# Kernel optimization log

Measured on AMD Instinct MI355X. Metric: run time of the kernel, lower is better.

The kernel has to match this reference:

```python
import jax, jax.numpy as jnp
import numpy as np

B, S, D = 4, 2048, 256
H, RANK, DFF = 8, 8, 1024
DK = D // H
EPS = 1e-5


def _linear(x, W, b):
    # torch nn.Linear: y = x @ W.T + b, W shape (out, in)
    return jnp.einsum('bsd,od->bso', x, W) + b


def _layer_norm(x, g, b):
    mu = jnp.mean(x, axis=-1, keepdims=True)
    var = jnp.var(x, axis=-1, keepdims=True)
    return (x - mu) * jax.lax.rsqrt(var + EPS) * g + b


def setup_inputs() -> dict:
    key = jax.random.key(0)
    ks = jax.random.split(key, 20)
    r = RANK * H
    s = lambda fan_in: 1.0 / np.sqrt(fan_in)
    inp = {
        'x': jax.random.normal(ks[0], (B, S, D), jnp.float32),
        'Wq_down': jax.random.uniform(ks[1], (r, D), jnp.float32, -s(D), s(D)),
        'bq_down': jnp.zeros((r,), jnp.float32),
        'Wq_up': jax.random.uniform(ks[2], (D, r), jnp.float32, -s(r), s(r)),
        'bq_up': jnp.zeros((D,), jnp.float32),
        'Wk_down': jax.random.uniform(ks[3], (r, D), jnp.float32, -s(D), s(D)),
        'bk_down': jnp.zeros((r,), jnp.float32),
        'Wk_up': jax.random.uniform(ks[4], (D, r), jnp.float32, -s(r), s(r)),
        'bk_up': jnp.zeros((D,), jnp.float32),
        'Wv': jax.random.uniform(ks[5], (D, D), jnp.float32, -s(D), s(D)),
        'bv': jnp.zeros((D,), jnp.float32),
        'Wo': jax.random.uniform(ks[6], (D, D), jnp.float32, -s(D), s(D)),
        'bo': jnp.zeros((D,), jnp.float32),
        'ln_attn_g': jnp.ones((D,), jnp.float32),
        'ln_attn_b': jnp.zeros((D,), jnp.float32),
        'W_ff1': jax.random.uniform(ks[7], (DFF, D), jnp.float32, -s(D), s(D)),
        'b_ff1': jnp.zeros((DFF,), jnp.float32),
        'W_ff2': jax.random.uniform(ks[8], (D, DFF), jnp.float32, -s(DFF), s(DFF)),
        'b_ff2': jnp.zeros((D,), jnp.float32),
        'ln_blk_g': jnp.ones((D,), jnp.float32),
        'ln_blk_b': jnp.zeros((D,), jnp.float32),
    }
    return inp


def reference(x, Wq_down, bq_down, Wq_up, bq_up, Wk_down, bk_down, Wk_up, bk_up,
              Wv, bv, Wo, bo, ln_attn_g, ln_attn_b,
              W_ff1, b_ff1, W_ff2, b_ff2, ln_blk_g, ln_blk_b):
    # Low-rank Q/K: down-project to rank*H then up-project to D
    Q = _linear(_linear(x, Wq_down, bq_down), Wq_up, bq_up)
    K = _linear(_linear(x, Wk_down, bk_down), Wk_up, bk_up)
    V = _linear(x, Wv, bv)
    # (B,S,D) -> (B,H,S,DK)
    Q = Q.reshape(B, S, H, DK).transpose(0, 2, 1, 3)
    K = K.reshape(B, S, H, DK).transpose(0, 2, 1, 3)
    V = V.reshape(B, S, H, DK).transpose(0, 2, 1, 3)
    scale = 1.0 / np.sqrt(DK).astype(np.float32)
    scores = jnp.einsum('bhqd,bhkd->bhqk', Q, K) * scale
    attn = jax.nn.softmax(scores, axis=-1)
    context = jnp.einsum('bhqk,bhkd->bhqd', attn, V)
    context = context.transpose(0, 2, 1, 3).reshape(B, S, D)
    attn_out = _linear(context, Wo, bo)
    attn_out = _layer_norm(x + attn_out, ln_attn_g, ln_attn_b)
    # FFN: Linear -> GELU (exact erf, torch default) -> Linear
    h = jax.nn.gelu(_linear(attn_out, W_ff1, b_ff1), approximate=False)
    ff = _linear(h, W_ff2, b_ff2)
    return _layer_norm(attn_out + ff, ln_blk_g, ln_blk_b)
```

## Files before the change

### kernel.cpp

```cpp
#include <hip/hip_runtime.h>
#include <hip/hip_bf16.h>
#include <math.h>

#define NB 4
#define NS 2048
#define ND 256
#define NH 8
#define NDK 32
#define NDFF 1024
#define NROWS (NB * NS)
#define KC 4
#define KVB 64
#define KTILES (NS / KC / KVB)

using short8 = __attribute__((ext_vector_type(8))) short;
using f32x4  = __attribute__((ext_vector_type(4))) float;

__device__ __forceinline__ unsigned short f2bf(float f) {
  union { float f; unsigned u; } v; v.f = f;
  unsigned r = v.u + 0x7fffu + ((v.u >> 16) & 1u);
  return (unsigned short)(r >> 16);
}
__device__ __forceinline__ float bf2f(unsigned short u) {
  union { unsigned u; float f; } v; v.u = ((unsigned)u) << 16;
  return v.f;
}
__device__ __forceinline__ unsigned cvt_pk_bf16(float lo, float hi) {
  unsigned r;
  asm("v_cvt_pk_bf16_f32 %0, %1, %2" : "=v"(r) : "v"(lo), "v"(hi));
  return r;
}
__device__ __forceinline__ void gl_lds16(const void* g, void* l) {
  __builtin_amdgcn_global_load_lds(
      (const __attribute__((address_space(1))) unsigned int*)g,
      (__attribute__((address_space(3))) unsigned int*)l, 16, 0, 0);
}

__global__ void cvt_batch(const float* s0, const float* s1, const float* s2,
                          const float* s3, const float* s4, const float* s5,
                          const float* s6, const float* s7, const float* s8,
                          unsigned short* d0, unsigned short* d1,
                          unsigned short* d2, unsigned short* d3,
                          unsigned short* d4, unsigned short* d5,
                          unsigned short* d6, unsigned short* d7,
                          unsigned short* d8,
                          int n0, int n1, int n2, int n3, int n4, int n5,
                          int n6, int n7, int n8) {
  const float* s; unsigned short* d; int n;
  switch (blockIdx.y) {
    case 0: s = s0; d = d0; n = n0; break;
    case 1: s = s1; d = d1; n = n1; break;
    case 2: s = s2; d = d2; n = n2; break;
    case 3: s = s3; d = d3; n = n3; break;
    case 4: s = s4; d = d4; n = n4; break;
    case 5: s = s5; d = d5; n = n5; break;
    case 6: s = s6; d = d6; n = n6; break;
    case 7: s = s7; d = d7; n = n7; break;
    default: s = s8; d = d8; n = n8; break;
  }
  for (int i = (blockIdx.x * 256 + threadIdx.x) * 4; i < n; i += 512 * 256 * 4) {
    float4 v = *reinterpret_cast<const float4*>(s + i);
    ushort4 o;
    o.x = f2bf(v.x); o.y = f2bf(v.y); o.z = f2bf(v.z); o.w = f2bf(v.w);
    *reinterpret_cast<ushort4*>(d + i) = o;
  }
}

template <int ACT, int OBF>
__global__ __launch_bounds__(256)
void gemm_nt(const unsigned short* __restrict__ A, int lda,
             const unsigned short* __restrict__ W,
             const float* __restrict__ bias, const float* __restrict__ bias2,
             int bsplit, void* __restrict__ outp, int K, int O) {
  __shared__ __align__(16) unsigned short lA[128 * 64];
  __shared__ __align__(16) unsigned short lB[64 * 64];
  const int tid = threadIdx.x, lane = tid & 63, wid = tid >> 6;
  const int wr = wid >> 1, wc = wid & 1;
  const int l15 = lane & 15, lg = lane >> 4;
  const int bm = blockIdx.x, bn = blockIdx.y;

  f32x4 acc[4][2];
#pragma unroll
  for (int i = 0; i < 4; ++i)
#pragma unroll
    for (int j = 0; j < 2; ++j) acc[i][j] = (f32x4)0.0f;

  for (int k0 = 0; k0 < K; k0 += 64) {
#pragma unroll
    for (int it = 0; it < 4; ++it) {
      int c = it * 256 + tid;
      int row = c >> 3, cc = (c & 7) ^ (row & 7);
      gl_lds16(A + (size_t)(bm * 128 + row) * lda + k0 + cc * 8, &lA[c * 8]);
    }
#pragma unroll
    for (int it = 0; it < 2; ++it) {
      int c = it * 256 + tid;
      int row = c >> 3, cc = (c & 7) ^ (row & 7);
      gl_lds16(W + (size_t)(bn * 64 + row) * K + k0 + cc * 8, &lB[c * 8]);
    }
    __syncthreads();
#pragma unroll
    for (int kk = 0; kk < 2; ++kk) {
      short8 a[4], b[2];
#pragma unroll
      for (int mf = 0; mf < 4; ++mf) {
        int row = wr * 64 + mf * 16 + l15;
        a[mf] = *reinterpret_cast<const short8*>(
            &lA[row * 64 + (((kk * 4 + lg) ^ (l15 & 7)) << 3)]);
      }
#pragma unroll
      for (int nf = 0; nf < 2; ++nf) {
        int row = wc * 32 + nf * 16 + l15;
        b[nf] = *reinterpret_cast<const short8*>(
            &lB[row * 64 + (((kk * 4 + lg) ^ (l15 & 7)) << 3)]);
      }
#pragma unroll
      for (int mf = 0; mf < 4; ++mf)
#pragma unroll
        for (int nf = 0; nf < 2; ++nf)
          acc[mf][nf] = __builtin_amdgcn_mfma_f32_16x16x32_bf16(
              a[mf], b[nf], acc[mf][nf], 0, 0, 0);
    }
    __syncthreads();
  }

#pragma unroll
  for (int mf = 0; mf < 4; ++mf)
#pragma unroll
    for (int nf = 0; nf < 2; ++nf) {
      int col = bn * 64 + wc * 32 + nf * 16 + l15;
      float bv = (bias2 && col >= bsplit) ? bias2[col - bsplit] : bias[col];
#pragma unroll
      for (int i = 0; i < 4; ++i) {
        int row = bm * 128 + wr * 64 + mf * 16 + lg * 4 + i;
        float v = acc[mf][nf][i] + bv;
        if (ACT == 1) v = 0.5f * v * (1.0f + erff(v * 0.70710678118654752f));
        if (OBF)
          ((unsigned short*)outp)[(size_t)row * O + col] = f2bf(v);
        else
          ((float*)outp)[(size_t)row * O + col] = v;
      }
    }
}

__global__ __launch_bounds__(256)
void attn_kernel(const unsigned short* __restrict__ Qb,
                 const unsigned short* __restrict__ Kb,
                 const unsigned short* __restrict__ Vb,
                 unsigned short* __restrict__ pacc,
                 float* __restrict__ pl) {
  __shared__ __align__(16) unsigned short lK[2][KVB * 32];
  __shared__ __align__(16) unsigned short lVt[2][32 * 72];
  __shared__ __align__(16) unsigned short lP[4][16 * 64];
  const int tid = threadIdx.x, lane = tid & 63, wid = tid >> 6;
  const int l15 = lane & 15, lg = lane >> 4;
  const int qt = blockIdx.x, bh = blockIdx.y, kc = blockIdx.z;
  const int b = bh >> 3, h = bh & 7;
  const size_t headoff = (size_t)h * NDK;
  const int qbase = qt * 128 + wid * 32;
  const int kv0 = kc * (NS / KC);
  const float qscale = 0.25508686f;

  short8 aq[2];
#pragma unroll
  for (int r = 0; r < 2; ++r) {
    short8 v = *reinterpret_cast<const short8*>(
        Qb + (size_t)(b * NS + qbase + r * 16 + l15) * ND + headoff + lg * 8);
#pragma unroll
    for (int j = 0; j < 8; ++j)
      v[j] = (short)f2bf(bf2f((unsigned short)v[j]) * qscale);
    aq[r] = v;
  }

  const unsigned short* kptr =
      Kb + (size_t)(b * NS + kv0 + (tid >> 2)) * ND + headoff + (tid & 3) * 8;
  const int vd0 = (tid & 15) * 2, vk0 = (tid >> 4) * 4;
  const unsigned short* vptr =
      Vb + (size_t)(b * NS + kv0 + vk0) * ND + headoff + vd0;
  const size_t kvstride = (size_t)KVB * ND;

  auto writeV = [&](const unsigned* w, int buf) {
    unsigned lo0 = (w[0] & 0xffffu) | (w[1] << 16);
    unsigned lo1 = (w[2] & 0xffffu) | (w[3] << 16);
    unsigned hi0 = (w[0] >> 16) | (w[1] & 0xffff0000u);
    unsigned hi1 = (w[2] >> 16) | (w[3] & 0xffff0000u);
    *reinterpret_cast<uint2*>(&lVt[buf][vd0 * 72 + vk0]) = make_uint2(lo0, lo1);
    *reinterpret_cast<uint2*>(&lVt[buf][(vd0 + 1) * 72 + vk0]) =
        make_uint2(hi0, hi1);
  };

  f32x4 accT[2][2];
#pragma unroll
  for (int r = 0; r < 2; ++r)
#pragma unroll
    for (int d = 0; d < 2; ++d) accT[r][d] = (f32x4)0.0f;
  float l[2] = {0.0f, 0.0f};

  unsigned vr[4];
  gl_lds16(kptr, &lK[0][tid * 8]);
#pragma unroll
  for (int u = 0; u < 4; ++u)
    vr[u] = *reinterpret_cast<const unsigned*>(vptr + (size_t)u * ND);
  writeV(vr, 0);
  __syncthreads();

  for (int kt = 0; kt < KTILES; ++kt) {
    const int cur = kt & 1, nxt = cur ^ 1;
    const bool pf = (kt + 1 < KTILES);
    if (pf) {
      kptr += kvstride;
      vptr += kvstride;
      gl_lds16(kptr, &lK[nxt][tid * 8]);
#pragma unroll
      for (int u = 0; u < 4; ++u)
        vr[u] = *reinterpret_cast<const unsigned*>(vptr + (size_t)u * ND);
    }

#pragma unroll
    for (int r = 0; r < 2; ++r) {
      f32x4 sT[4];
      __builtin_amdgcn_s_setprio(1);
#pragma unroll
      for (int t = 0; t < 4; ++t) {
        short8 bk = *reinterpret_cast<const short8*>(
            &lK[cur][(t * 16 + l15) * 32 + lg * 8]);
        sT[t] = __builtin_amdgcn_mfma_f32_16x16x32_bf16(
            bk, aq[r], (f32x4)0.0f, 0, 0, 0);
      }
      __builtin_amdgcn_s_setprio(0);
#pragma unroll
      for (int t = 0; t < 4; ++t) {
        float p0 = __builtin_amdgcn_exp2f(sT[t][0]);
        float p1 = __builtin_amdgcn_exp2f(sT[t][1]);
        float p2 = __builtin_amdgcn_exp2f(sT[t][2]);
        float p3 = __builtin_amdgcn_exp2f(sT[t][3]);
        l[r] += (p0 + p1) + (p2 + p3);
        unsigned w0 = cvt_pk_bf16(p0, p1);
        unsigned w1 = cvt_pk_bf16(p2, p3);
        int blk = (t << 1) | (lg >> 1);
        *reinterpret_cast<uint2*>(
            &lP[wid][l15 * 64 + ((blk ^ (l15 & 7)) << 3) + ((lg & 1) << 2)]) =
            make_uint2(w0, w1);
      }
      __builtin_amdgcn_s_setprio(1);
#pragma unroll
      for (int kk = 0; kk < 2; ++kk) {
        short8 pa = *reinterpret_cast<const short8*>(
            &lP[wid][l15 * 64 + (((kk * 4 + lg) ^ (l15 & 7)) << 3)]);
#pragma unroll
        for (int dt = 0; dt < 2; ++dt) {
          short8 bv = *reinterpret_cast<const short8*>(
              &lVt[cur][(dt * 16 + l15) * 72 + kk * 32 + lg * 8]);
          accT[r][dt] = __builtin_amdgcn_mfma_f32_16x16x32_bf16(
              bv, pa, accT[r][dt], 0, 0, 0);
        }
      }
      __builtin_amdgcn_s_setprio(0);
    }

    if (pf) writeV(vr, nxt);
    __syncthreads();
  }

#pragma unroll
  for (int r = 0; r < 2; ++r) {
    l[r] += __shfl_xor(l[r], 16);
    l[r] += __shfl_xor(l[r], 32);
  }

#pragma unroll
  for (int r = 0; r < 2; ++r) {
    int qg = qbase + r * 16 + l15;
    size_t rowbase = ((size_t)kc * 65536 + (size_t)bh * NS + qg) * 32;
#pragma unroll
    for (int dt = 0; dt < 2; ++dt) {
      unsigned w0 = cvt_pk_bf16(accT[r][dt][0], accT[r][dt][1]);
      unsigned w1 = cvt_pk_bf16(accT[r][dt][2], accT[r][dt][3]);
      *reinterpret_cast<uint2*>(&pacc[rowbase + dt * 16 + lg * 4]) =
          make_uint2(w0, w1);
    }
  }
  if (lane < 16) {
#pragma unroll
    for (int r = 0; r < 2; ++r) {
      int qg = qbase + r * 16 + l15;
      pl[(size_t)kc * 65536 + (size_t)bh * NS + qg] = l[r];
    }
  }
}

__global__ __launch_bounds__(256)
void attn_combine(const unsigned short* __restrict__ pacc,
                  const float* __restrict__ pl,
                  unsigned short* __restrict__ ctx) {
  int gid = blockIdx.x * 256 + threadIdx.x;
  int r = gid >> 2, d8 = (gid & 3) * 8;
  float L = 0.0f;
#pragma unroll
  for (int c = 0; c < 4; ++c) L += pl[(size_t)c * 65536 + r];
  float inv = 1.0f / L;
  float o[8];
#pragma unroll
  for (int j = 0; j < 8; ++j) o[j] = 0.0f;
#pragma unroll
  for (int c = 0; c < 4; ++c) {
    short8 a = *reinterpret_cast<const short8*>(
        &pacc[((size_t)c * 65536 + r) * 32 + d8]);
#pragma unroll
    for (int j = 0; j < 8; ++j) o[j] += bf2f((unsigned short)a[j]);
  }
  int bh = r >> 11, q = r & 2047;
  int b = bh >> 3, h = bh & 7;
  short8 out;
#pragma unroll
  for (int j = 0; j < 8; ++j) out[j] = (short)f2bf(o[j] * inv);
  *reinterpret_cast<short8*>(
      &ctx[((size_t)(b * NS + q)) * ND + h * 32 + d8]) = out;
}

__global__ __launch_bounds__(256)
void ln_res_kernel(const float* __restrict__ a, const float* bsrc,
                   const float* __restrict__ g, const float* __restrict__ be,
                   float* yf, unsigned short* yb) {
  int row = blockIdx.x * 4 + (threadIdx.x >> 6);
  int lane = threadIdx.x & 63;
  size_t off = (size_t)row * ND + lane * 4;
  float4 va = *reinterpret_cast<const float4*>(a + off);
  float4 vb = *reinterpret_cast<const float4*>(bsrc + off);
  float v0 = va.x + vb.x, v1 = va.y + vb.y, v2 = va.z + vb.z, v3 = va.w + vb.w;
  float s = v0 + v1 + v2 + v3;
  float sq = v0 * v0 + v1 * v1 + v2 * v2 + v3 * v3;
#pragma unroll
  for (int o = 1; o < 64; o <<= 1) {
    s += __shfl_xor(s, o);
    sq += __shfl_xor(sq, o);
  }
  float mu = s * (1.0f / 256.0f);
  float var = sq * (1.0f / 256.0f) - mu * mu;
  float rs = rsqrtf(var + 1e-5f);
  float4 vg = *reinterpret_cast<const float4*>(g + lane * 4);
  float4 vbe = *reinterpret_cast<const float4*>(be + lane * 4);
  float o0 = (v0 - mu) * rs * vg.x + vbe.x;
  float o1 = (v1 - mu) * rs * vg.y + vbe.y;
  float o2 = (v2 - mu) * rs * vg.z + vbe.z;
  float o3 = (v3 - mu) * rs * vg.w + vbe.w;
  if (yf) *reinterpret_cast<float4*>(yf + off) = make_float4(o0, o1, o2, o3);
  if (yb) {
    ushort4 ob;
    ob.x = f2bf(o0); ob.y = f2bf(o1); ob.z = f2bf(o2); ob.w = f2bf(o3);
    *reinterpret_cast<ushort4*>(yb + off) = ob;
  }
}

extern "C" void kernel_launch(void* const* d_in, const int* in_sizes, int n_in,
                              void* d_out, int out_size, void* d_ws,
                              size_t ws_size, hipStream_t stream) {
  (void)in_sizes; (void)n_in; (void)out_size; (void)ws_size;
  const float* x   = (const float*)d_in[0];
  const float* Wqd = (const float*)d_in[1];
  const float* bqd = (const float*)d_in[2];
  const float* Wqu = (const float*)d_in[3];
  const float* bqu = (const float*)d_in[4];
  const float* Wkd = (const float*)d_in[5];
  const float* bkd = (const float*)d_in[6];
  const float* Wku = (const float*)d_in[7];
  const float* bku = (const float*)d_in[8];
  const float* Wv  = (const float*)d_in[9];
  const float* bv  = (const float*)d_in[10];
  const float* Wo  = (const float*)d_in[11];
  const float* bo  = (const float*)d_in[12];
  const float* g1  = (const float*)d_in[13];
  const float* be1 = (const float*)d_in[14];
  const float* Wf1 = (const float*)d_in[15];
  const float* bf1 = (const float*)d_in[16];
  const float* Wf2 = (const float*)d_in[17];
  const float* bf2 = (const float*)d_in[18];
  const float* g2  = (const float*)d_in[19];
  const float* be2 = (const float*)d_in[20];

  char* p = (char*)d_ws;
  auto alloc = [&](size_t bytes) {
    char* r = p;
    p += (bytes + 255) & ~(size_t)255;
    return r;
  };
  unsigned short* xb   = (unsigned short*)alloc((size_t)NROWS * ND * 2);
  unsigned short* wqkd = (unsigned short*)alloc(128 * 256 * 2);
  unsigned short* wqu  = (unsigned short*)alloc(256 * 64 * 2);
  unsigned short* wku  = (unsigned short*)alloc(256 * 64 * 2);
  unsigned short* wv   = (unsigned short*)alloc(256 * 256 * 2);
  unsigned short* wo   = (unsigned short*)alloc(256 * 256 * 2);
  unsigned short* wf1  = (unsigned short*)alloc(1024 * 256 * 2);
  unsigned short* wf2  = (unsigned short*)alloc(256 * 1024 * 2);
  unsigned short* qkd  = (unsigned short*)alloc((size_t)NROWS * 128 * 2);
  unsigned short* Qb   = (unsigned short*)alloc((size_t)NROWS * ND * 2);
  unsigned short* Kb   = (unsigned short*)alloc((size_t)NROWS * ND * 2);
  unsigned short* Vb   = (unsigned short*)alloc((size_t)NROWS * ND * 2);
  unsigned short* ctx  = (unsigned short*)alloc((size_t)NROWS * ND * 2);
  float*          y1   = (float*)alloc((size_t)NROWS * ND * 4);
  unsigned short* y1b  = (unsigned short*)alloc((size_t)NROWS * ND * 2);
  unsigned short* hb   = (unsigned short*)alloc((size_t)NROWS * NDFF * 2);
  float* ao = (float*)d_out;

  unsigned short* pacc = hb;
  float* pl = y1;

  cvt_batch<<<dim3(512, 9), 256, 0, stream>>>(
      x, Wqd, Wkd, Wqu, Wku, Wv, Wo, Wf1, Wf2,
      xb, wqkd, wqkd + 64 * 256, wqu, wku, wv, wo, wf1, wf2,
      NROWS * ND, 64 * 256, 64 * 256, 256 * 64, 256 * 64, 256 * 256,
      256 * 256, 1024 * 256, 256 * 1024);

  gemm_nt<0, 1><<<dim3(64, 2), 256, 0, stream>>>(
      xb, 256, wqkd, bqd, bkd, 64, qkd, 256, 128);
  gemm_nt<0, 1><<<dim3(64, 4), 256, 0, stream>>>(
      qkd, 128, wqu, bqu, nullptr, 0, Qb, 64, 256);
  gemm_nt<0, 1><<<dim3(64, 4), 256, 0, stream>>>(
      qkd + 64, 128, wku, bku, nullptr, 0, Kb, 64, 256);
  gemm_nt<0, 1><<<dim3(64, 4), 256, 0, stream>>>(
      xb, 256, wv, bv, nullptr, 0, Vb, 256, 256);

  attn_kernel<<<dim3(NS / 128, NB * NH, KC), 256, 0, stream>>>(
      Qb, Kb, Vb, pacc, pl);
  attn_combine<<<dim3(1024), 256, 0, stream>>>(pacc, pl, ctx);

  gemm_nt<0, 0><<<dim3(64, 4), 256, 0, stream>>>(
      ctx, 256, wo, bo, nullptr, 0, ao, 256, 256);
  ln_res_kernel<<<NROWS / 4, 256, 0, stream>>>(x, ao, g1, be1, y1, y1b);

  gemm_nt<1, 1><<<dim3(64, 16), 256, 0, stream>>>(
      y1b, 256, wf1, bf1, nullptr, 0, hb, 256, NDFF);
  gemm_nt<0, 0><<<dim3(64, 4), 256, 0, stream>>>(
      hb, 1024, wf2, bf2, nullptr, 0, ao, 1024, 256);
  ln_res_kernel<<<NROWS / 4, 256, 0, stream>>>(y1, ao, g2, be2,
                                               (float*)d_out, nullptr);
}
```

Measured before the change: 117.1 us.

## Double-buffer GEMM LDS, shrink M tiles, fuse residual, halve attention KV split

The GEMM kernel gets double-buffered LDS staging, so the next K tile's loads are issued while the current tile's MFMAs run, and a templated M tile size. Most GEMMs now use 64-row tiles, doubling the block count for better CU fill. The residual add moves into the GEMM epilogue, so the layer-norm kernel reads one tensor instead of two. The attention KV split drops from 4 to 2 chunks, which halves the partial-result traffic in the combine step but also halves the number of attention blocks. The double buffers use more LDS per block and may reduce occupancy.

```diff
diff --git a/kernel.cpp b/kernel.cpp
--- a/kernel.cpp
+++ b/kernel.cpp
@@ -9,7 +9,7 @@
 #define NDK 32
 #define NDFF 1024
 #define NROWS (NB * NS)
-#define KC 4
+#define KC 2
 #define KVB 64
 #define KTILES (NS / KC / KVB)
 
@@ -66,56 +66,66 @@
   }
 }
 
-template <int ACT, int OBF>
+template <int BM, int ACT, int OBF, int RES>
 __global__ __launch_bounds__(256)
 void gemm_nt(const unsigned short* __restrict__ A, int lda,
              const unsigned short* __restrict__ W,
              const float* __restrict__ bias, const float* __restrict__ bias2,
-             int bsplit, void* __restrict__ outp, int K, int O) {
-  __shared__ __align__(16) unsigned short lA[128 * 64];
-  __shared__ __align__(16) unsigned short lB[64 * 64];
+             int bsplit, const float* __restrict__ resid,
+             void* __restrict__ outp, int K, int O) {
+  constexpr int MFW = BM / 32;
+  __shared__ __align__(16) unsigned short lA[2][BM * 64];
+  __shared__ __align__(16) unsigned short lB[2][64 * 64];
   const int tid = threadIdx.x, lane = tid & 63, wid = tid >> 6;
   const int wr = wid >> 1, wc = wid & 1;
   const int l15 = lane & 15, lg = lane >> 4;
   const int bm = blockIdx.x, bn = blockIdx.y;
 
-  f32x4 acc[4][2];
-#pragma unroll
-  for (int i = 0; i < 4; ++i)
-#pragma unroll
-    for (int j = 0; j < 2; ++j) acc[i][j] = (f32x4)0.0f;
-
-  for (int k0 = 0; k0 < K; k0 += 64) {
-#pragma unroll
-    for (int it = 0; it < 4; ++it) {
+  auto stage = [&](int k0, int buf) {
+#pragma unroll
+    for (int it = 0; it < BM / 32; ++it) {
       int c = it * 256 + tid;
       int row = c >> 3, cc = (c & 7) ^ (row & 7);
-      gl_lds16(A + (size_t)(bm * 128 + row) * lda + k0 + cc * 8, &lA[c * 8]);
+      gl_lds16(A + (size_t)(bm * BM + row) * lda + k0 + cc * 8,
+               &lA[buf][c * 8]);
     }
 #pragma unroll
     for (int it = 0; it < 2; ++it) {
       int c = it * 256 + tid;
       int row = c >> 3, cc = (c & 7) ^ (row & 7);
-      gl_lds16(W + (size_t)(bn * 64 + row) * K + k0 + cc * 8, &lB[c * 8]);
-    }
-    __syncthreads();
+      gl_lds16(W + (size_t)(bn * 64 + row) * K + k0 + cc * 8, &lB[buf][c * 8]);
+    }
+  };
+
+  f32x4 acc[MFW][2];
+#pragma unroll
+  for (int i = 0; i < MFW; ++i)
+#pragma unroll
+    for (int j = 0; j < 2; ++j) acc[i][j] = (f32x4)0.0f;
+
+  const int T = K >> 6;
+  stage(0, 0);
+  __syncthreads();
+  for (int t = 0; t < T; ++t) {
+    const int cur = t & 1;
+    if (t + 1 < T) stage((t + 1) << 6, cur ^ 1);
 #pragma unroll
     for (int kk = 0; kk < 2; ++kk) {
-      short8 a[4], b[2];
-#pragma unroll
-      for (int mf = 0; mf < 4; ++mf) {
-        int row = wr * 64 + mf * 16 + l15;
+      short8 a[MFW], b[2];
+#pragma unroll
+      for (int mf = 0; mf < MFW; ++mf) {
+        int row = wr * (BM / 2) + mf * 16 + l15;
         a[mf] = *reinterpret_cast<const short8*>(
-            &lA[row * 64 + (((kk * 4 + lg) ^ (l15 & 7)) << 3)]);
+            &lA[cur][row * 64 + (((kk * 4 + lg) ^ (l15 & 7)) << 3)]);
       }
 #pragma unroll
       for (int nf = 0; nf < 2; ++nf) {
         int row = wc * 32 + nf * 16 + l15;
         b[nf] = *reinterpret_cast<const short8*>(
-            &lB[row * 64 + (((kk * 4 + lg) ^ (l15 & 7)) << 3)]);
-      }
-#pragma unroll
-      for (int mf = 0; mf < 4; ++mf)
+            &lB[cur][row * 64 + (((kk * 4 + lg) ^ (l15 & 7)) << 3)]);
+      }
+#pragma unroll
+      for (int mf = 0; mf < MFW; ++mf)
 #pragma unroll
         for (int nf = 0; nf < 2; ++nf)
           acc[mf][nf] = __builtin_amdgcn_mfma_f32_16x16x32_bf16(
@@ -125,16 +135,17 @@
   }
 
 #pragma unroll
-  for (int mf = 0; mf < 4; ++mf)
+  for (int mf = 0; mf < MFW; ++mf)
 #pragma unroll
     for (int nf = 0; nf < 2; ++nf) {
       int col = bn * 64 + wc * 32 + nf * 16 + l15;
       float bv = (bias2 && col >= bsplit) ? bias2[col - bsplit] : bias[col];
 #pragma unroll
       for (int i = 0; i < 4; ++i) {
-        int row = bm * 128 + wr * 64 + mf * 16 + lg * 4 + i;
+        int row = bm * BM + wr * (BM / 2) + mf * 16 + lg * 4 + i;
         float v = acc[mf][nf][i] + bv;
         if (ACT == 1) v = 0.5f * v * (1.0f + erff(v * 0.70710678118654752f));
+        if (RES) v += resid[(size_t)row * O + col];
         if (OBF)
           ((unsigned short*)outp)[(size_t)row * O + col] = f2bf(v);
         else
@@ -297,13 +308,13 @@
   int r = gid >> 2, d8 = (gid & 3) * 8;
   float L = 0.0f;
 #pragma unroll
-  for (int c = 0; c < 4; ++c) L += pl[(size_t)c * 65536 + r];
+  for (int c = 0; c < KC; ++c) L += pl[(size_t)c * 65536 + r];
   float inv = 1.0f / L;
   float o[8];
 #pragma unroll
   for (int j = 0; j < 8; ++j) o[j] = 0.0f;
 #pragma unroll
-  for (int c = 0; c < 4; ++c) {
+  for (int c = 0; c < KC; ++c) {
     short8 a = *reinterpret_cast<const short8*>(
         &pacc[((size_t)c * 65536 + r) * 32 + d8]);
 #pragma unroll
@@ -326,8 +337,11 @@
   int lane = threadIdx.x & 63;
   size_t off = (size_t)row * ND + lane * 4;
   float4 va = *reinterpret_cast<const float4*>(a + off);
-  float4 vb = *reinterpret_cast<const float4*>(bsrc + off);
-  float v0 = va.x + vb.x, v1 = va.y + vb.y, v2 = va.z + vb.z, v3 = va.w + vb.w;
+  float v0 = va.x, v1 = va.y, v2 = va.z, v3 = va.w;
+  if (bsrc) {
+    float4 vb = *reinterpret_cast<const float4*>(bsrc + off);
+    v0 += vb.x; v1 += vb.y; v2 += vb.z; v3 += vb.w;
+  }
   float s = v0 + v1 + v2 + v3;
   float sq = v0 * v0 + v1 * v1 + v2 * v2 + v3 * v3;
 #pragma unroll
@@ -411,27 +425,27 @@
       NROWS * ND, 64 * 256, 64 * 256, 256 * 64, 256 * 64, 256 * 256,
       256 * 256, 1024 * 256, 256 * 1024);
 
-  gemm_nt<0, 1><<<dim3(64, 2), 256, 0, stream>>>(
-      xb, 256, wqkd, bqd, bkd, 64, qkd, 256, 128);
-  gemm_nt<0, 1><<<dim3(64, 4), 256, 0, stream>>>(
-      qkd, 128, wqu, bqu, nullptr, 0, Qb, 64, 256);
-  gemm_nt<0, 1><<<dim3(64, 4), 256, 0, stream>>>(
-      qkd + 64, 128, wku, bku, nullptr, 0, Kb, 64, 256);
-  gemm_nt<0, 1><<<dim3(64, 4), 256, 0, stream>>>(
-      xb, 256, wv, bv, nullptr, 0, Vb, 256, 256);
+  gemm_nt<64, 0, 1, 0><<<dim3(128, 2), 256, 0, stream>>>(
+      xb, 256, wqkd, bqd, bkd, 64, nullptr, qkd, 256, 128);
+  gemm_nt<64, 0, 1, 0><<<dim3(128, 4), 256, 0, stream>>>(
+      qkd, 128, wqu, bqu, nullptr, 0, nullptr, Qb, 64, 256);
+  gemm_nt<64, 0, 1, 0><<<dim3(128, 4), 256, 0, stream>>>(
+      qkd + 64, 128, wku, bku, nullptr, 0, nullptr, Kb, 64, 256);
+  gemm_nt<64, 0, 1, 0><<<dim3(128, 4), 256, 0, stream>>>(
+      xb, 256, wv, bv, nullptr, 0, nullptr, Vb, 256, 256);
 
   attn_kernel<<<dim3(NS / 128, NB * NH, KC), 256, 0, stream>>>(
       Qb, Kb, Vb, pacc, pl);
   attn_combine<<<dim3(1024), 256, 0, stream>>>(pacc, pl, ctx);
 
-  gemm_nt<0, 0><<<dim3(64, 4), 256, 0, stream>>>(
-      ctx, 256, wo, bo, nullptr, 0, ao, 256, 256);
-  ln_res_kernel<<<NROWS / 4, 256, 0, stream>>>(x, ao, g1, be1, y1, y1b);
-
-  gemm_nt<1, 1><<<dim3(64, 16), 256, 0, stream>>>(
-      y1b, 256, wf1, bf1, nullptr, 0, hb, 256, NDFF);
-  gemm_nt<0, 0><<<dim3(64, 4), 256, 0, stream>>>(
-      hb, 1024, wf2, bf2, nullptr, 0, ao, 1024, 256);
-  ln_res_kernel<<<NROWS / 4, 256, 0, stream>>>(y1, ao, g2, be2,
+  gemm_nt<64, 0, 0, 1><<<dim3(128, 4), 256, 0, stream>>>(
+      ctx, 256, wo, bo, nullptr, 0, x, ao, 256, 256);
+  ln_res_kernel<<<NROWS / 4, 256, 0, stream>>>(ao, nullptr, g1, be1, y1, y1b);
+
+  gemm_nt<128, 1, 1, 0><<<dim3(64, 16), 256, 0, stream>>>(
+      y1b, 256, wf1, bf1, nullptr, 0, nullptr, hb, 256, NDFF);
+  gemm_nt<64, 0, 0, 1><<<dim3(128, 4), 256, 0, stream>>>(
+      hb, 1024, wf2, bf2, nullptr, 0, y1, ao, 1024, 256);
+  ln_res_kernel<<<NROWS / 4, 256, 0, stream>>>(ao, nullptr, g2, be2,
                                                (float*)d_out, nullptr);
 }
```

Result: no change. 116.0 us (-0.9%).
